# Performance work log

Measured on AMD Instinct MI355X. Metric: run time of the kernel, lower is better.

## Reference

```python
import jax, jax.numpy as jnp
import numpy as np

B, T = 64, 2048          # batch, encoder max steps
E, A, P = 256, 128, 128  # embedding_dim, attention_dim, prenet_dim
R, D, H = 1024, 1024, 256  # attention_rnn_dim, decoder_rnn_dim, hidden_dim
F, K = 32, 31            # location n_filters, kernel_size
PAD = (K - 1) // 2
NEG_INF = -1e30  # stands in for -inf; softmax-safe in fp32/bf16


def lstm_cell(x, h, c, W_ih, W_hh, b_ih, b_hh):
    # torch.nn.LSTMCell gate order: i, f, g, o
    gates = x @ W_ih.T + h @ W_hh.T + (b_ih + b_hh)
    i, f, g, o = jnp.split(gates, 4, axis=-1)
    c2 = jax.nn.sigmoid(f) * c + jax.nn.sigmoid(i) * jnp.tanh(g)
    h2 = jax.nn.sigmoid(o) * jnp.tanh(c2)
    return h2, c2


def setup_inputs() -> dict:
    key = jax.random.key(0)
    ks = jax.random.split(key, 30)
    n = jax.random.normal
    s = 0.02  # weight scale
    inp = {
        "last_frame": n(ks[0], (B, P)),
        "att_h": n(ks[1], (B, R)) * 0.1,
        "att_c": n(ks[2], (B, R)) * 0.1,
        "att_w": jax.random.uniform(ks[3], (B, T)) / T,
        "att_w_cum": jax.random.uniform(ks[4], (B, T)),
        "att_ctx": n(ks[5], (B, E)) * 0.1,
        "dec_h": n(ks[6], (B, D)) * 0.1,
        "dec_c": n(ks[7], (B, D)) * 0.1,
        "memory": n(ks[8], (B, T, E)),
        "processed_memory": n(ks[9], (B, T, A)) * 0.1,
        # attention LSTMCell (input = embedding_dim + prenet_dim = 384)
        "W_ih_a": n(ks[10], (4 * R, E + P)) * s,
        "W_hh_a": n(ks[11], (4 * R, R)) * s,
        "b_ih_a": n(ks[12], (4 * R,)) * s,
        "b_hh_a": n(ks[13], (4 * R,)) * s,
        # attention layer
        "W_q": n(ks[14], (A, R)) * s,
        "W_v": n(ks[15], (1, A)) * s,
        "W_loc": n(ks[16], (F, 2, K)) * s,   # Conv1d(2 -> F, k=31), no bias
        "W_lfc": n(ks[17], (A, F)) * s,
        # decoder LSTMCell (input = attention_rnn_dim + embedding_dim = 1280)
        "W_ih_d": n(ks[18], (4 * D, R + E)) * s,
        "W_hh_d": n(ks[19], (4 * D, D)) * s,
        "b_ih_d": n(ks[20], (4 * D,)) * s,
        "b_hh_d": n(ks[21], (4 * D,)) * s,
        # output heads
        "W_proj": n(ks[22], (H, D + E)) * s,
        "b_proj": n(ks[23], (H,)) * s,
        "W_gate": n(ks[24], (1, D + E)) * s,
        "b_gate": n(ks[25], (1,)) * s,
        "mask": jax.random.randint(ks[26], (B, T), 0, 2).astype(bool),
    }
    return inp


def reference(last_frame, att_h, att_c, att_w, att_w_cum, att_ctx, dec_h, dec_c,
              memory, processed_memory,
              W_ih_a, W_hh_a, b_ih_a, b_hh_a,
              W_q, W_v, W_loc, W_lfc,
              W_ih_d, W_hh_d, b_ih_d, b_hh_d,
              W_proj, b_proj, W_gate, b_gate, mask):
    # ---- attention RNN step (dropout = identity at eval) ----
    attention_in = jnp.concatenate([last_frame, att_ctx], axis=-1)  # [B, P+E]
    ah, ac = lstm_cell(attention_in, att_h, att_c, W_ih_a, W_hh_a, b_ih_a, b_hh_a)

    # ---- location-sensitive attention ----
    aw_cat = jnp.stack([att_w, att_w_cum], axis=1)  # [B, 2, T]
    loc = jax.lax.conv_general_dilated(
        aw_cat, W_loc, window_strides=(1,), padding=[(PAD, PAD)],
        dimension_numbers=('NCH', 'OIH', 'NCH'))  # [B, F, T]
    loc = jnp.einsum('bft,af->bta', loc, W_lfc)    # LocationLayer fc, [B, T, A]

    pq = (ah @ W_q.T)[:, None, :]                   # processed query [B, 1, A]
    energies = jnp.tanh(pq + processed_memory + loc) @ W_v[0]  # [B, T]
    energies = jnp.where(mask, NEG_INF, energies)
    weights = jax.nn.softmax(energies, axis=1)      # [B, T]
    ctx = jnp.einsum('bt,bte->be', weights, memory)  # [B, E]

    # ---- decoder RNN step ----
    decoder_in = jnp.concatenate([ah, ctx], axis=-1)  # [B, R+E]
    dh, dc = lstm_cell(decoder_in, dec_h, dec_c, W_ih_d, W_hh_d, b_ih_d, b_hh_d)

    dhac = jnp.concatenate([dh, ctx], axis=1)         # [B, D+E]
    decoder_output = dhac @ W_proj.T + b_proj          # [B, H]
    stop_prediction = dhac @ W_gate.T + b_gate         # [B, 1]
    return decoder_output, stop_prediction, weights[:, None, :]  # [B, 1, T]
```

## Files before the change

### kernel.cpp

```cpp
#include <hip/hip_runtime.h>
#include <stdint.h>

typedef unsigned short u16;
typedef __attribute__((ext_vector_type(8))) u16 u16x8;
typedef __attribute__((ext_vector_type(8))) __bf16 bf16x8;
typedef __attribute__((ext_vector_type(4))) float f32x4;

#define L2E 1.4426950408889634f

__device__ __forceinline__ float bf2f(u16 u) {
  union { unsigned i; float f; } v; v.i = ((unsigned)u) << 16; return v.f;
}
__device__ __forceinline__ u16 f2bf_rne(float f) {
  union { float f; unsigned u; } v; v.f = f;
  const unsigned r = v.u + 0x7FFFu + ((v.u >> 16) & 1u);
  return (u16)(r >> 16);
}
__device__ __forceinline__ bf16x8 ldb(const u16* p) {
  u16x8 v = *reinterpret_cast<const u16x8*>(p);
  return __builtin_bit_cast(bf16x8, v);
}
__device__ __forceinline__ void split8t(const float* p, bf16x8& h, bf16x8& l) {
  const float4 v0 = *reinterpret_cast<const float4*>(p);
  const float4 v1 = *reinterpret_cast<const float4*>(p + 4);
  const float f[8] = {v0.x, v0.y, v0.z, v0.w, v1.x, v1.y, v1.z, v1.w};
  u16x8 hu, lu;
#pragma unroll
  for (int i = 0; i < 8; ++i) {
    union { float f; unsigned u; } a; a.f = f[i];
    hu[i] = (u16)(a.u >> 16);
    union { float f; unsigned u; } hf; hf.u = a.u & 0xFFFF0000u;
    union { float f; unsigned u; } lo; lo.f = f[i] - hf.f;
    lu[i] = (u16)(lo.u >> 16);
  }
  h = __builtin_bit_cast(bf16x8, hu);
  l = __builtin_bit_cast(bf16x8, lu);
}
__device__ __forceinline__ f32x4 mfma16(bf16x8 a, bf16x8 b, f32x4 c) {
  return __builtin_amdgcn_mfma_f32_16x16x32_bf16(a, b, c, 0, 0, 0);
}
__device__ __forceinline__ float sigm(float x) {
  return 1.0f / (1.0f + exp2f(-L2E * x));
}
__device__ __forceinline__ float tanh_(float x) {
  return 1.0f - 2.0f / (1.0f + exp2f(2.0f * L2E * x));
}

__global__ __launch_bounds__(128) void k0_prep(
    const float* __restrict__ Wloc, const float* __restrict__ Wlfc,
    u16* __restrict__ w2b)
{
  const int k = blockIdx.x, a = threadIdx.x;
  float v = 0.0f;
  if (k < 62) {
    const int c = (k >= 31) ? 1 : 0, dk = k - c * 31;
    for (int f = 0; f < 32; ++f)
      v += Wlfc[a * 32 + f] * Wloc[f * 62 + c * 31 + dk];
  }
  w2b[a * 64 + k] = f2bf_rne(v);
}

#define KSA 8
__global__ __launch_bounds__(256) void k1_gemm(
    const float* __restrict__ lf, const float* __restrict__ actx,
    const float* __restrict__ ah_in,
    const float* __restrict__ Wih, const float* __restrict__ Whh,
    float* __restrict__ gates)
{
  const int tid = threadIdx.x;
  const int g = tid >> 6, lane = tid & 63, quad = lane >> 4, l16 = lane & 15;
  const int jb = blockIdx.x * 16, ks = blockIdx.y;
  const int n = g * 1024 + jb + l16;
  const int s0 = (ks * 44) / KSA, s1 = ((ks + 1) * 44) / KSA;
  f32x4 acc[4] = {{0,0,0,0},{0,0,0,0},{0,0,0,0},{0,0,0,0}};
  for (int s = s0; s < s1; ++s) {
    const int kb = s * 32, k = kb + quad * 8;
    const float* bp = (k < 384) ? (Wih + n * 384 + k) : (Whh + n * 1024 + (k - 384));
    bf16x8 b_h, b_l; split8t(bp, b_h, b_l);
#pragma unroll
    for (int mt = 0; mt < 4; ++mt) {
      const int mA = mt * 16 + l16;
      const float* ap;
      if (k < 128)      ap = lf    + mA * 128  + k;
      else if (k < 384) ap = actx  + mA * 256  + (k - 128);
      else              ap = ah_in + mA * 1024 + (k - 384);
      bf16x8 a_h, a_l; split8t(ap, a_h, a_l);
      acc[mt] = mfma16(a_h, b_h, acc[mt]);
      acc[mt] = mfma16(a_h, b_l, acc[mt]);
      acc[mt] = mfma16(a_l, b_h, acc[mt]);
    }
  }
#pragma unroll
  for (int mt = 0; mt < 4; ++mt)
#pragma unroll
    for (int r = 0; r < 4; ++r)
      atomicAdd(&gates[(mt * 16 + quad * 4 + r) * 4096 + n], acc[mt][r]);
}

__global__ __launch_bounds__(256) void k1_epi(
    const float* __restrict__ gates, const float* __restrict__ ac_in,
    const float* __restrict__ bih, const float* __restrict__ bhh,
    float* __restrict__ ah_f, u16* __restrict__ xd)
{
  const int lin = blockIdx.x * 256 + threadIdx.x;
  const int m = lin >> 10, j = lin & 1023;
  const float pi = gates[m * 4096 + j]        + bih[j]        + bhh[j];
  const float pf = gates[m * 4096 + 1024 + j] + bih[1024 + j] + bhh[1024 + j];
  const float pg = gates[m * 4096 + 2048 + j] + bih[2048 + j] + bhh[2048 + j];
  const float po = gates[m * 4096 + 3072 + j] + bih[3072 + j] + bhh[3072 + j];
  const float c2 = sigm(pf) * ac_in[m * 1024 + j] + sigm(pi) * tanh_(pg);
  const float h2 = sigm(po) * tanh_(c2);
  ah_f[m * 1024 + j] = h2;
  xd[m * 1280 + j]   = f2bf_rne(h2);
}

__global__ __launch_bounds__(256) void k2a_pq(
    const float* __restrict__ ah_f, const float* __restrict__ Wq, float* __restrict__ pq)
{
  const int lane = threadIdx.x & 63;
  const int wid = blockIdx.x * 4 + (threadIdx.x >> 6);
  const int a = wid & 127, bg = wid >> 7;
  float s[4] = {0, 0, 0, 0};
  for (int k = lane; k < 1024; k += 64) {
    const float wq = Wq[a * 1024 + k];
#pragma unroll
    for (int i = 0; i < 4; ++i) s[i] += wq * ah_f[(bg * 4 + i) * 1024 + k];
  }
#pragma unroll
  for (int i = 0; i < 4; ++i) {
    float v = s[i];
    for (int off = 1; off < 64; off <<= 1) v += __shfl_xor(v, off, 64);
    if (lane == 0) pq[(bg * 4 + i) * 128 + a] = v;
  }
}

__global__ __launch_bounds__(256) void k2_energy(
    const float* __restrict__ aw, const float* __restrict__ awc,
    const float* __restrict__ pm, const float* __restrict__ Wv,
    const float* __restrict__ pq, const u16* __restrict__ w2b,
    const int* __restrict__ msk, float* __restrict__ e_g)
{
  __shared__ __align__(16) u16 awin[2][64];
  __shared__ __align__(16) u16 pms[32 * 128];
  __shared__ __align__(16) u16 w2s[128 * 64];
  __shared__ float wvs[128];
  __shared__ float pqs[128];
  __shared__ float es[32];
  const int b = blockIdx.y, t0 = blockIdx.x * 32, tid = threadIdx.x;

  if (tid < 128) {
    const int c = tid >> 6, ii = tid & 63;
    const int t = t0 - 15 + ii;
    float v = 0.0f;
    if (ii < 62 && t >= 0 && t < 2048) v = (c ? awc : aw)[b * 2048 + t];
    awin[c][ii] = f2bf_rne(v);
    wvs[tid] = Wv[tid];
    pqs[tid] = pq[b * 128 + tid];
  }
  if (tid < 32) es[tid] = 0.0f;
  {
    const float* src = pm + (size_t)b * 262144 + (size_t)t0 * 128;
    const int i = tid * 16;
#pragma unroll
    for (int q = 0; q < 4; ++q) {
      const float4 v = *reinterpret_cast<const float4*>(&src[i + q * 4]);
      pms[i + q * 4 + 0] = f2bf_rne(v.x);
      pms[i + q * 4 + 1] = f2bf_rne(v.y);
      pms[i + q * 4 + 2] = f2bf_rne(v.z);
      pms[i + q * 4 + 3] = f2bf_rne(v.w);
    }
  }
  {
    const int i = tid * 32;
#pragma unroll
    for (int q = 0; q < 4; ++q)
      *reinterpret_cast<u16x8*>(&w2s[i + q * 8]) = *reinterpret_cast<const u16x8*>(&w2b[i + q * 8]);
  }
  __syncthreads();

  const int w = tid >> 6, lane = tid & 63, quad = lane >> 4, l16 = lane & 15;
  const int mt = w & 1, ng = w >> 1;
  f32x4 acc[4] = {{0,0,0,0},{0,0,0,0},{0,0,0,0},{0,0,0,0}};
#pragma unroll
  for (int ksx = 0; ksx < 2; ++ksx) {
    bf16x8 af;
    const int m = mt * 16 + l16;
#pragma unroll
    for (int jj = 0; jj < 8; ++jj) {
      const int k = ksx * 32 + quad * 8 + jj;
      u16 v = 0;
      if (k < 62) { const int c = (k >= 31) ? 1 : 0; const int dk = k - c * 31; v = awin[c][m + dk]; }
      af[jj] = __builtin_bit_cast(__bf16, v);
    }
#pragma unroll
    for (int p = 0; p < 4; ++p) {
      const int a = (ng * 4 + p) * 16 + l16;
      bf16x8 bfr = *reinterpret_cast<const bf16x8*>(&w2s[a * 64 + ksx * 32 + quad * 8]);
      acc[p] = mfma16(af, bfr, acc[p]);
    }
  }
#pragma unroll
  for (int r = 0; r < 4; ++r) {
    const int tl = mt * 16 + quad * 4 + r;
    float part = 0.0f;
#pragma unroll
    for (int p = 0; p < 4; ++p) {
      const int a = (ng * 4 + p) * 16 + l16;
      const float x = pqs[a] + bf2f(pms[tl * 128 + a]) + acc[p][r];
      part += wvs[a] * tanh_(x);
    }
    part += __shfl_xor(part, 1, 64);
    part += __shfl_xor(part, 2, 64);
    part += __shfl_xor(part, 4, 64);
    part += __shfl_xor(part, 8, 64);
    if (l16 == 0) atomicAdd(&es[tl], part);
  }
  __syncthreads();
  if (tid < 32) {
    const int t = t0 + tid;
    e_g[b * 2048 + t] = msk[b * 2048 + t] ? -1e30f : es[tid];
  }
}

__global__ __launch_bounds__(256) void k3a_softmax(
    const float* __restrict__ e_g, float* __restrict__ w_f, float* __restrict__ out_w)
{
  const int b = blockIdx.x, tid = threadIdx.x;
  __shared__ float red[4];
  float v[8];
  float mx = -3.0e38f;
#pragma unroll
  for (int i = 0; i < 8; ++i) { v[i] = e_g[b * 2048 + tid + i * 256]; mx = fmaxf(mx, v[i]); }
  for (int off = 1; off < 64; off <<= 1) mx = fmaxf(mx, __shfl_xor(mx, off, 64));
  if ((tid & 63) == 0) red[tid >> 6] = mx;
  __syncthreads();
  mx = fmaxf(fmaxf(red[0], red[1]), fmaxf(red[2], red[3]));
  float ex[8], s = 0.0f;
#pragma unroll
  for (int i = 0; i < 8; ++i) { ex[i] = exp2f((v[i] - mx) * L2E); s += ex[i]; }
  for (int off = 1; off < 64; off <<= 1) s += __shfl_xor(s, off, 64);
  __syncthreads();
  if ((tid & 63) == 0) red[tid >> 6] = s;
  __syncthreads();
  const float rs = 1.0f / (red[0] + red[1] + red[2] + red[3]);
#pragma unroll
  for (int i = 0; i < 8; ++i) {
    const int t = tid + i * 256;
    const float wv = ex[i] * rs;
    w_f[b * 2048 + t]   = wv;
    out_w[b * 2048 + t] = wv;
  }
}

__global__ __launch_bounds__(256) void k3b_ctx(
    const float* __restrict__ w_f, const float* __restrict__ mem, float* __restrict__ ctx)
{
  const int b = blockIdx.y, tc = blockIdx.x, tid = threadIdx.x;
  const int w = tid >> 6, lane = tid & 63;
  __shared__ float wsm[256];
  __shared__ float red[4][256];
  wsm[tid] = w_f[b * 2048 + tc * 256 + tid];
  __syncthreads();
  const float* mp = mem + (size_t)b * 524288 + ((size_t)tc * 256 + w * 64) * 256 + lane * 4;
  f32x4 acc = {0, 0, 0, 0};
#pragma unroll 4
  for (int t = 0; t < 64; ++t) {
    const float wt = wsm[w * 64 + t];
    const float4 v = *reinterpret_cast<const float4*>(mp + (size_t)t * 256);
    acc[0] += wt * v.x; acc[1] += wt * v.y; acc[2] += wt * v.z; acc[3] += wt * v.w;
  }
#pragma unroll
  for (int i = 0; i < 4; ++i) red[w][lane * 4 + i] = acc[i];
  __syncthreads();
  const float s = red[0][tid] + red[1][tid] + red[2][tid] + red[3][tid];
  atomicAdd(&ctx[b * 256 + tid], s);
}

__global__ __launch_bounds__(256) void k3c_cvt(
    const float* __restrict__ ctx, u16* __restrict__ xd, u16* __restrict__ dhac)
{
  const int b = blockIdx.x, e = threadIdx.x;
  const u16 v = f2bf_rne(ctx[b * 256 + e]);
  xd[b * 1280 + 1024 + e]   = v;
  dhac[b * 1280 + 1024 + e] = v;
}

__global__ __launch_bounds__(256) void k4_gemm(
    const u16* __restrict__ xd, const float* __restrict__ dh_in,
    const float* __restrict__ Wih, const float* __restrict__ Whh,
    float* __restrict__ gates)
{
  const int tid = threadIdx.x;
  const int g = tid >> 6, lane = tid & 63, quad = lane >> 4, l16 = lane & 15;
  const int jb = blockIdx.x * 16, ks = blockIdx.y;
  const int n = g * 1024 + jb + l16;
  const int kb0 = ks * 256, kb1 = kb0 + 256;
  f32x4 acc[4] = {{0,0,0,0},{0,0,0,0},{0,0,0,0},{0,0,0,0}};
  for (int kb = kb0; kb < kb1; kb += 32) {
    const int k = kb + quad * 8;
    const float* bp = (k < 1280) ? (Wih + n * 1280 + k) : (Whh + n * 1024 + (k - 1280));
    bf16x8 b_h, b_l; split8t(bp, b_h, b_l);
    if (k < 1280) {
#pragma unroll
      for (int mt = 0; mt < 4; ++mt) {
        bf16x8 a_h = ldb(xd + (mt * 16 + l16) * 1280 + k);
        acc[mt] = mfma16(a_h, b_h, acc[mt]);
        acc[mt] = mfma16(a_h, b_l, acc[mt]);
      }
    } else {
#pragma unroll
      for (int mt = 0; mt < 4; ++mt) {
        bf16x8 a_h, a_l; split8t(dh_in + (mt * 16 + l16) * 1024 + (k - 1280), a_h, a_l);
        acc[mt] = mfma16(a_h, b_h, acc[mt]);
        acc[mt] = mfma16(a_h, b_l, acc[mt]);
        acc[mt] = mfma16(a_l, b_h, acc[mt]);
      }
    }
  }
#pragma unroll
  for (int mt = 0; mt < 4; ++mt)
#pragma unroll
    for (int r = 0; r < 4; ++r)
      atomicAdd(&gates[(mt * 16 + quad * 4 + r) * 4096 + n], acc[mt][r]);
}

__global__ __launch_bounds__(256) void k4_epi(
    const float* __restrict__ gates, const float* __restrict__ dc_in,
    const float* __restrict__ bih, const float* __restrict__ bhh,
    u16* __restrict__ dhac)
{
  const int lin = blockIdx.x * 256 + threadIdx.x;
  const int m = lin >> 10, j = lin & 1023;
  const float pi = gates[m * 4096 + j]        + bih[j]        + bhh[j];
  const float pf = gates[m * 4096 + 1024 + j] + bih[1024 + j] + bhh[1024 + j];
  const float pg = gates[m * 4096 + 2048 + j] + bih[2048 + j] + bhh[2048 + j];
  const float po = gates[m * 4096 + 3072 + j] + bih[3072 + j] + bhh[3072 + j];
  const float c2 = sigm(pf) * dc_in[m * 1024 + j] + sigm(pi) * tanh_(pg);
  const float h2 = sigm(po) * tanh_(c2);
  dhac[m * 1280 + j] = f2bf_rne(h2);
}

__global__ __launch_bounds__(256) void k5_gemm(
    const u16* __restrict__ dhac, const float* __restrict__ Wp,
    float* __restrict__ proj)
{
  const int tid = threadIdx.x;
  const int w = tid >> 6, lane = tid & 63, quad = lane >> 4, l16 = lane & 15;
  const int n = blockIdx.x * 64 + w * 16 + l16, ks = blockIdx.y;
  const int kb0 = ks * 64;
  f32x4 acc[4] = {{0,0,0,0},{0,0,0,0},{0,0,0,0},{0,0,0,0}};
#pragma unroll
  for (int kb = kb0; kb < kb0 + 64; kb += 32) {
    const int k = kb + quad * 8;
    bf16x8 b_h, b_l; split8t(Wp + n * 1280 + k, b_h, b_l);
#pragma unroll
    for (int mt = 0; mt < 4; ++mt) {
      bf16x8 af = ldb(dhac + (mt * 16 + l16) * 1280 + k);
      acc[mt] = mfma16(af, b_h, acc[mt]);
      acc[mt] = mfma16(af, b_l, acc[mt]);
    }
  }
#pragma unroll
  for (int mt = 0; mt < 4; ++mt)
#pragma unroll
    for (int r = 0; r < 4; ++r)
      atomicAdd(&proj[(mt * 16 + quad * 4 + r) * 256 + n], acc[mt][r]);
}

__global__ __launch_bounds__(256) void k5_epi(
    const float* __restrict__ proj, const float* __restrict__ bp,
    const u16* __restrict__ dhac, const float* __restrict__ Wg,
    const float* __restrict__ bg, float* __restrict__ out)
{
  const int tid = threadIdx.x;
  if (blockIdx.x < 64) {
    const int m = blockIdx.x;
    out[m * 256 + tid] = proj[m * 256 + tid] + bp[tid];
  } else {
    const int w = tid >> 6, lane = tid & 63;
    const int bb = (blockIdx.x - 64) * 4 + w;
    float s = 0.0f;
    for (int k = lane; k < 1280; k += 64) s += bf2f(dhac[bb * 1280 + k]) * Wg[k];
    for (int off = 1; off < 64; off <<= 1) s += __shfl_xor(s, off, 64);
    if (lane == 0) out[16384 + bb] = s + bg[0];
  }
}

extern "C" void kernel_launch(void* const* d_in, const int* in_sizes, int n_in,
                              void* d_out, int out_size, void* d_ws, size_t ws_size,
                              hipStream_t stream)
{
  const float* lf    = (const float*)d_in[0];
  const float* ah0   = (const float*)d_in[1];
  const float* ac0   = (const float*)d_in[2];
  const float* aw    = (const float*)d_in[3];
  const float* awc   = (const float*)d_in[4];
  const float* actx  = (const float*)d_in[5];
  const float* dh0   = (const float*)d_in[6];
  const float* dc0   = (const float*)d_in[7];
  const float* mem   = (const float*)d_in[8];
  const float* pm    = (const float*)d_in[9];
  const float* Wih_a = (const float*)d_in[10];
  const float* Whh_a = (const float*)d_in[11];
  const float* bih_a = (const float*)d_in[12];
  const float* bhh_a = (const float*)d_in[13];
  const float* Wq    = (const float*)d_in[14];
  const float* Wv    = (const float*)d_in[15];
  const float* Wloc  = (const float*)d_in[16];
  const float* Wlfc  = (const float*)d_in[17];
  const float* Wih_d = (const float*)d_in[18];
  const float* Whh_d = (const float*)d_in[19];
  const float* bih_d = (const float*)d_in[20];
  const float* bhh_d = (const float*)d_in[21];
  const float* Wp    = (const float*)d_in[22];
  const float* bp    = (const float*)d_in[23];
  const float* Wg    = (const float*)d_in[24];
  const float* bg    = (const float*)d_in[25];
  const int* msk     = (const int*)d_in[26];

  float* wsf     = (float*)d_ws;
  float* gates_a = wsf;
  float* gates_d = wsf + 262144;
  float* proj    = wsf + 524288;
  float* ctx     = wsf + 540672;
  float* ah_f    = wsf + 557056;
  float* pq      = wsf + 622592;
  float* e_g     = wsf + 630784;
  float* w_f     = wsf + 761856;
  u16*  xd       = (u16*)(wsf + 892928);
  u16*  dhac     = xd + 81920;
  u16*  w2b      = dhac + 81920;

  float* out   = (float*)d_out;
  float* out_w = out + 16448;

  hipMemsetAsync(d_ws, 0, 557056 * sizeof(float), stream);

  k0_prep    <<<64, 128, 0, stream>>>(Wloc, Wlfc, w2b);
  k1_gemm    <<<dim3(64, KSA), 256, 0, stream>>>(lf, actx, ah0, Wih_a, Whh_a, gates_a);
  k1_epi     <<<256, 256, 0, stream>>>(gates_a, ac0, bih_a, bhh_a, ah_f, xd);
  k2a_pq     <<<512, 256, 0, stream>>>(ah_f, Wq, pq);
  k2_energy  <<<dim3(64, 64), 256, 0, stream>>>(aw, awc, pm, Wv, pq, w2b, msk, e_g);
  k3a_softmax<<<64, 256, 0, stream>>>(e_g, w_f, out_w);
  k3b_ctx    <<<dim3(8, 64), 256, 0, stream>>>(w_f, mem, ctx);
  k3c_cvt    <<<64, 256, 0, stream>>>(ctx, xd, dhac);
  k4_gemm    <<<dim3(64, 9), 256, 0, stream>>>(xd, dh0, Wih_d, Whh_d, gates_d);
  k4_epi     <<<256, 256, 0, stream>>>(gates_d, dc0, bih_d, bhh_d, dhac);
  k5_gemm    <<<dim3(4, 20), 256, 0, stream>>>(dhac, Wp, proj);
  k5_epi     <<<80, 256, 0, stream>>>(proj, bp, dhac, Wg, bg, out);
}
```

Measured before the change: 400.3 us.

## Fuse all decoder stages into one cooperative persistent kernel with grid barriers

Replaces the twelve separate launches and the memset with a single cooperative persistent kernel. Stages are separated by a software grid barrier, and the workspace is zeroed inside the kernel. The decoder GEMM now converts ctx to bf16 inline, and the xd layout is shrunk. This removes per-launch overhead and the gaps between kernels. In exchange, occupancy is limited by the union of all shared-memory buffers, and grid-strided loops may leave some stages with fewer blocks than before, such as the energy stage's 4096 blocks.

```diff
diff --git a/kernel.cpp b/kernel.cpp
--- a/kernel.cpp
+++ b/kernel.cpp
@@ -7,6 +7,7 @@
 typedef __attribute__((ext_vector_type(4))) float f32x4;
 
 #define L2E 1.4426950408889634f
+#define NBLK_MAX 512
 
 __device__ __forceinline__ float bf2f(u16 u) {
   union { unsigned i; float f; } v; v.i = ((unsigned)u) << 16; return v.f;
@@ -36,6 +37,15 @@
   h = __builtin_bit_cast(bf16x8, hu);
   l = __builtin_bit_cast(bf16x8, lu);
 }
+__device__ __forceinline__ bf16x8 cvt8_rne(const float* p) {
+  const float4 v0 = *reinterpret_cast<const float4*>(p);
+  const float4 v1 = *reinterpret_cast<const float4*>(p + 4);
+  const float f[8] = {v0.x, v0.y, v0.z, v0.w, v1.x, v1.y, v1.z, v1.w};
+  u16x8 u;
+#pragma unroll
+  for (int i = 0; i < 8; ++i) u[i] = f2bf_rne(f[i]);
+  return __builtin_bit_cast(bf16x8, u);
+}
 __device__ __forceinline__ f32x4 mfma16(bf16x8 a, bf16x8 b, f32x4 c) {
   return __builtin_amdgcn_mfma_f32_16x16x32_bf16(a, b, c, 0, 0, 0);
 }
@@ -46,343 +56,362 @@
   return 1.0f - 2.0f / (1.0f + exp2f(2.0f * L2E * x));
 }
 
-__global__ __launch_bounds__(128) void k0_prep(
-    const float* __restrict__ Wloc, const float* __restrict__ Wlfc,
-    u16* __restrict__ w2b)
+__device__ __align__(128) unsigned g_cnt = 0;
+__device__ __align__(128) unsigned g_gen = 0;
+
+__device__ __forceinline__ void gbar() {
+  __syncthreads();
+  if (threadIdx.x == 0) {
+    const unsigned tgt = gridDim.x;
+    const unsigned g = __hip_atomic_load(&g_gen, __ATOMIC_RELAXED, __HIP_MEMORY_SCOPE_AGENT);
+    const unsigned a = __hip_atomic_fetch_add(&g_cnt, 1u, __ATOMIC_ACQ_REL, __HIP_MEMORY_SCOPE_AGENT);
+    if (a == tgt - 1u) {
+      __hip_atomic_store(&g_cnt, 0u, __ATOMIC_RELAXED, __HIP_MEMORY_SCOPE_AGENT);
+      __hip_atomic_store(&g_gen, g + 1u, __ATOMIC_RELEASE, __HIP_MEMORY_SCOPE_AGENT);
+    } else {
+      while (__hip_atomic_load(&g_gen, __ATOMIC_RELAXED, __HIP_MEMORY_SCOPE_AGENT) == g)
+        __builtin_amdgcn_s_sleep(2);
+      (void)__hip_atomic_load(&g_gen, __ATOMIC_ACQUIRE, __HIP_MEMORY_SCOPE_AGENT);
+    }
+  }
+  __syncthreads();
+}
+
+struct MArgs {
+  const float *lf, *ah0, *ac0, *aw, *awc, *actx, *dh0, *dc0, *mem, *pm;
+  const float *Wih_a, *Whh_a, *bih_a, *bhh_a;
+  const float *Wq, *Wv, *Wloc, *Wlfc;
+  const float *Wih_d, *Whh_d, *bih_d, *bhh_d;
+  const float *Wp, *bp, *Wg, *bg;
+  const int *msk;
+  float *wsf;
+  float *out;
+};
+
+__global__ __launch_bounds__(256, 2) void mega(MArgs A)
 {
-  const int k = blockIdx.x, a = threadIdx.x;
-  float v = 0.0f;
-  if (k < 62) {
-    const int c = (k >= 31) ? 1 : 0, dk = k - c * 31;
-    for (int f = 0; f < 32; ++f)
-      v += Wlfc[a * 32 + f] * Wloc[f * 62 + c * 31 + dk];
-  }
-  w2b[a * 64 + k] = f2bf_rne(v);
-}
-
-#define KSA 8
-__global__ __launch_bounds__(256) void k1_gemm(
-    const float* __restrict__ lf, const float* __restrict__ actx,
-    const float* __restrict__ ah_in,
-    const float* __restrict__ Wih, const float* __restrict__ Whh,
-    float* __restrict__ gates)
-{
-  const int tid = threadIdx.x;
-  const int g = tid >> 6, lane = tid & 63, quad = lane >> 4, l16 = lane & 15;
-  const int jb = blockIdx.x * 16, ks = blockIdx.y;
-  const int n = g * 1024 + jb + l16;
-  const int s0 = (ks * 44) / KSA, s1 = ((ks + 1) * 44) / KSA;
-  f32x4 acc[4] = {{0,0,0,0},{0,0,0,0},{0,0,0,0},{0,0,0,0}};
-  for (int s = s0; s < s1; ++s) {
-    const int kb = s * 32, k = kb + quad * 8;
-    const float* bp = (k < 384) ? (Wih + n * 384 + k) : (Whh + n * 1024 + (k - 384));
-    bf16x8 b_h, b_l; split8t(bp, b_h, b_l);
-#pragma unroll
-    for (int mt = 0; mt < 4; ++mt) {
-      const int mA = mt * 16 + l16;
-      const float* ap;
-      if (k < 128)      ap = lf    + mA * 128  + k;
-      else if (k < 384) ap = actx  + mA * 256  + (k - 128);
-      else              ap = ah_in + mA * 1024 + (k - 384);
-      bf16x8 a_h, a_l; split8t(ap, a_h, a_l);
-      acc[mt] = mfma16(a_h, b_h, acc[mt]);
-      acc[mt] = mfma16(a_h, b_l, acc[mt]);
-      acc[mt] = mfma16(a_l, b_h, acc[mt]);
-    }
-  }
-#pragma unroll
-  for (int mt = 0; mt < 4; ++mt)
-#pragma unroll
-    for (int r = 0; r < 4; ++r)
-      atomicAdd(&gates[(mt * 16 + quad * 4 + r) * 4096 + n], acc[mt][r]);
-}
-
-__global__ __launch_bounds__(256) void k1_epi(
-    const float* __restrict__ gates, const float* __restrict__ ac_in,
-    const float* __restrict__ bih, const float* __restrict__ bhh,
-    float* __restrict__ ah_f, u16* __restrict__ xd)
-{
-  const int lin = blockIdx.x * 256 + threadIdx.x;
-  const int m = lin >> 10, j = lin & 1023;
-  const float pi = gates[m * 4096 + j]        + bih[j]        + bhh[j];
-  const float pf = gates[m * 4096 + 1024 + j] + bih[1024 + j] + bhh[1024 + j];
-  const float pg = gates[m * 4096 + 2048 + j] + bih[2048 + j] + bhh[2048 + j];
-  const float po = gates[m * 4096 + 3072 + j] + bih[3072 + j] + bhh[3072 + j];
-  const float c2 = sigm(pf) * ac_in[m * 1024 + j] + sigm(pi) * tanh_(pg);
-  const float h2 = sigm(po) * tanh_(c2);
-  ah_f[m * 1024 + j] = h2;
-  xd[m * 1280 + j]   = f2bf_rne(h2);
-}
-
-__global__ __launch_bounds__(256) void k2a_pq(
-    const float* __restrict__ ah_f, const float* __restrict__ Wq, float* __restrict__ pq)
-{
-  const int lane = threadIdx.x & 63;
-  const int wid = blockIdx.x * 4 + (threadIdx.x >> 6);
-  const int a = wid & 127, bg = wid >> 7;
-  float s[4] = {0, 0, 0, 0};
-  for (int k = lane; k < 1024; k += 64) {
-    const float wq = Wq[a * 1024 + k];
-#pragma unroll
-    for (int i = 0; i < 4; ++i) s[i] += wq * ah_f[(bg * 4 + i) * 1024 + k];
-  }
-#pragma unroll
-  for (int i = 0; i < 4; ++i) {
-    float v = s[i];
-    for (int off = 1; off < 64; off <<= 1) v += __shfl_xor(v, off, 64);
-    if (lane == 0) pq[(bg * 4 + i) * 128 + a] = v;
-  }
-}
-
-__global__ __launch_bounds__(256) void k2_energy(
-    const float* __restrict__ aw, const float* __restrict__ awc,
-    const float* __restrict__ pm, const float* __restrict__ Wv,
-    const float* __restrict__ pq, const u16* __restrict__ w2b,
-    const int* __restrict__ msk, float* __restrict__ e_g)
-{
+  const int tid  = threadIdx.x;
+  const int bid  = blockIdx.x;
+  const int gd   = gridDim.x;
+  const int gtid = bid * 256 + tid;
+  const int gs   = gd * 256;
+  const int w    = tid >> 6, lane = tid & 63, quad = lane >> 4, l16 = lane & 15;
+
+  float* gates_a = A.wsf;
+  float* gates_d = A.wsf + 262144;
+  float* proj    = A.wsf + 524288;
+  float* ctx     = A.wsf + 540672;
+  float* ah_f    = A.wsf + 557056;
+  float* pq      = A.wsf + 622592;
+  float* e_g     = A.wsf + 630784;
+  u16*  xd       = (u16*)(A.wsf + 761856);
+  u16*  dhac     = (u16*)(A.wsf + 794624);
+  u16*  w2b      = (u16*)(A.wsf + 835584);
+  float* out     = A.out;
+  float* out_w   = A.out + 16448;
+
   __shared__ __align__(16) u16 awin[2][64];
   __shared__ __align__(16) u16 pms[32 * 128];
   __shared__ __align__(16) u16 w2s[128 * 64];
   __shared__ float wvs[128];
   __shared__ float pqs[128];
   __shared__ float es[32];
-  const int b = blockIdx.y, t0 = blockIdx.x * 32, tid = threadIdx.x;
-
-  if (tid < 128) {
-    const int c = tid >> 6, ii = tid & 63;
-    const int t = t0 - 15 + ii;
-    float v = 0.0f;
-    if (ii < 62 && t >= 0 && t < 2048) v = (c ? awc : aw)[b * 2048 + t];
-    awin[c][ii] = f2bf_rne(v);
-    wvs[tid] = Wv[tid];
-    pqs[tid] = pq[b * 128 + tid];
-  }
-  if (tid < 32) es[tid] = 0.0f;
+  __shared__ float red4[4];
+  __shared__ float wsm[256];
+  __shared__ float redc[4][256];
+
   {
-    const float* src = pm + (size_t)b * 262144 + (size_t)t0 * 128;
-    const int i = tid * 16;
-#pragma unroll
-    for (int q = 0; q < 4; ++q) {
-      const float4 v = *reinterpret_cast<const float4*>(&src[i + q * 4]);
-      pms[i + q * 4 + 0] = f2bf_rne(v.x);
-      pms[i + q * 4 + 1] = f2bf_rne(v.y);
-      pms[i + q * 4 + 2] = f2bf_rne(v.z);
-      pms[i + q * 4 + 3] = f2bf_rne(v.w);
-    }
-  }
-  {
-    const int i = tid * 32;
-#pragma unroll
-    for (int q = 0; q < 4; ++q)
-      *reinterpret_cast<u16x8*>(&w2s[i + q * 8]) = *reinterpret_cast<const u16x8*>(&w2b[i + q * 8]);
-  }
-  __syncthreads();
-
-  const int w = tid >> 6, lane = tid & 63, quad = lane >> 4, l16 = lane & 15;
-  const int mt = w & 1, ng = w >> 1;
-  f32x4 acc[4] = {{0,0,0,0},{0,0,0,0},{0,0,0,0},{0,0,0,0}};
-#pragma unroll
-  for (int ksx = 0; ksx < 2; ++ksx) {
-    bf16x8 af;
-    const int m = mt * 16 + l16;
-#pragma unroll
-    for (int jj = 0; jj < 8; ++jj) {
-      const int k = ksx * 32 + quad * 8 + jj;
-      u16 v = 0;
-      if (k < 62) { const int c = (k >= 31) ? 1 : 0; const int dk = k - c * 31; v = awin[c][m + dk]; }
-      af[jj] = __builtin_bit_cast(__bf16, v);
-    }
-#pragma unroll
-    for (int p = 0; p < 4; ++p) {
-      const int a = (ng * 4 + p) * 16 + l16;
-      bf16x8 bfr = *reinterpret_cast<const bf16x8*>(&w2s[a * 64 + ksx * 32 + quad * 8]);
-      acc[p] = mfma16(af, bfr, acc[p]);
-    }
-  }
-#pragma unroll
-  for (int r = 0; r < 4; ++r) {
-    const int tl = mt * 16 + quad * 4 + r;
-    float part = 0.0f;
-#pragma unroll
-    for (int p = 0; p < 4; ++p) {
-      const int a = (ng * 4 + p) * 16 + l16;
-      const float x = pqs[a] + bf2f(pms[tl * 128 + a]) + acc[p][r];
-      part += wvs[a] * tanh_(x);
-    }
-    part += __shfl_xor(part, 1, 64);
-    part += __shfl_xor(part, 2, 64);
-    part += __shfl_xor(part, 4, 64);
-    part += __shfl_xor(part, 8, 64);
-    if (l16 == 0) atomicAdd(&es[tl], part);
-  }
-  __syncthreads();
-  if (tid < 32) {
-    const int t = t0 + tid;
-    e_g[b * 2048 + t] = msk[b * 2048 + t] ? -1e30f : es[tid];
-  }
-}
-
-__global__ __launch_bounds__(256) void k3a_softmax(
-    const float* __restrict__ e_g, float* __restrict__ w_f, float* __restrict__ out_w)
-{
-  const int b = blockIdx.x, tid = threadIdx.x;
-  __shared__ float red[4];
-  float v[8];
-  float mx = -3.0e38f;
-#pragma unroll
-  for (int i = 0; i < 8; ++i) { v[i] = e_g[b * 2048 + tid + i * 256]; mx = fmaxf(mx, v[i]); }
-  for (int off = 1; off < 64; off <<= 1) mx = fmaxf(mx, __shfl_xor(mx, off, 64));
-  if ((tid & 63) == 0) red[tid >> 6] = mx;
-  __syncthreads();
-  mx = fmaxf(fmaxf(red[0], red[1]), fmaxf(red[2], red[3]));
-  float ex[8], s = 0.0f;
-#pragma unroll
-  for (int i = 0; i < 8; ++i) { ex[i] = exp2f((v[i] - mx) * L2E); s += ex[i]; }
-  for (int off = 1; off < 64; off <<= 1) s += __shfl_xor(s, off, 64);
-  __syncthreads();
-  if ((tid & 63) == 0) red[tid >> 6] = s;
-  __syncthreads();
-  const float rs = 1.0f / (red[0] + red[1] + red[2] + red[3]);
-#pragma unroll
-  for (int i = 0; i < 8; ++i) {
-    const int t = tid + i * 256;
-    const float wv = ex[i] * rs;
-    w_f[b * 2048 + t]   = wv;
-    out_w[b * 2048 + t] = wv;
-  }
-}
-
-__global__ __launch_bounds__(256) void k3b_ctx(
-    const float* __restrict__ w_f, const float* __restrict__ mem, float* __restrict__ ctx)
-{
-  const int b = blockIdx.y, tc = blockIdx.x, tid = threadIdx.x;
-  const int w = tid >> 6, lane = tid & 63;
-  __shared__ float wsm[256];
-  __shared__ float red[4][256];
-  wsm[tid] = w_f[b * 2048 + tc * 256 + tid];
-  __syncthreads();
-  const float* mp = mem + (size_t)b * 524288 + ((size_t)tc * 256 + w * 64) * 256 + lane * 4;
-  f32x4 acc = {0, 0, 0, 0};
-#pragma unroll 4
-  for (int t = 0; t < 64; ++t) {
-    const float wt = wsm[w * 64 + t];
-    const float4 v = *reinterpret_cast<const float4*>(mp + (size_t)t * 256);
-    acc[0] += wt * v.x; acc[1] += wt * v.y; acc[2] += wt * v.z; acc[3] += wt * v.w;
-  }
-#pragma unroll
-  for (int i = 0; i < 4; ++i) red[w][lane * 4 + i] = acc[i];
-  __syncthreads();
-  const float s = red[0][tid] + red[1][tid] + red[2][tid] + red[3][tid];
-  atomicAdd(&ctx[b * 256 + tid], s);
-}
-
-__global__ __launch_bounds__(256) void k3c_cvt(
-    const float* __restrict__ ctx, u16* __restrict__ xd, u16* __restrict__ dhac)
-{
-  const int b = blockIdx.x, e = threadIdx.x;
-  const u16 v = f2bf_rne(ctx[b * 256 + e]);
-  xd[b * 1280 + 1024 + e]   = v;
-  dhac[b * 1280 + 1024 + e] = v;
-}
-
-__global__ __launch_bounds__(256) void k4_gemm(
-    const u16* __restrict__ xd, const float* __restrict__ dh_in,
-    const float* __restrict__ Wih, const float* __restrict__ Whh,
-    float* __restrict__ gates)
-{
-  const int tid = threadIdx.x;
-  const int g = tid >> 6, lane = tid & 63, quad = lane >> 4, l16 = lane & 15;
-  const int jb = blockIdx.x * 16, ks = blockIdx.y;
-  const int n = g * 1024 + jb + l16;
-  const int kb0 = ks * 256, kb1 = kb0 + 256;
-  f32x4 acc[4] = {{0,0,0,0},{0,0,0,0},{0,0,0,0},{0,0,0,0}};
-  for (int kb = kb0; kb < kb1; kb += 32) {
-    const int k = kb + quad * 8;
-    const float* bp = (k < 1280) ? (Wih + n * 1280 + k) : (Whh + n * 1024 + (k - 1280));
-    bf16x8 b_h, b_l; split8t(bp, b_h, b_l);
-    if (k < 1280) {
+    f32x4* z = (f32x4*)A.wsf;
+    for (int i = gtid; i < 139264; i += gs) z[i] = (f32x4){0.f, 0.f, 0.f, 0.f};
+    for (int lin = gtid; lin < 8192; lin += gs) {
+      const int a = lin >> 6, k = lin & 63;
+      float v = 0.0f;
+      if (k < 62) {
+        const int c = (k >= 31) ? 1 : 0, dk = k - c * 31;
+        for (int f = 0; f < 32; ++f)
+          v += A.Wlfc[a * 32 + f] * A.Wloc[f * 62 + c * 31 + dk];
+      }
+      w2b[a * 64 + k] = f2bf_rne(v);
+    }
+  }
+  gbar();
+
+  for (int vb = bid; vb < 512; vb += gd) {
+    const int g = w;
+    const int jt = vb & 63, ks = vb >> 6;
+    const int n = g * 1024 + jt * 16 + l16;
+    const int s0 = (ks * 44) / 8, s1 = ((ks + 1) * 44) / 8;
+    f32x4 acc[4] = {{0,0,0,0},{0,0,0,0},{0,0,0,0},{0,0,0,0}};
+    for (int s = s0; s < s1; ++s) {
+      const int kb = s * 32, k = kb + quad * 8;
+      const float* bp = (k < 384) ? (A.Wih_a + n * 384 + k) : (A.Whh_a + n * 1024 + (k - 384));
+      bf16x8 b_h, b_l; split8t(bp, b_h, b_l);
 #pragma unroll
       for (int mt = 0; mt < 4; ++mt) {
-        bf16x8 a_h = ldb(xd + (mt * 16 + l16) * 1280 + k);
-        acc[mt] = mfma16(a_h, b_h, acc[mt]);
-        acc[mt] = mfma16(a_h, b_l, acc[mt]);
-      }
-    } else {
-#pragma unroll
-      for (int mt = 0; mt < 4; ++mt) {
-        bf16x8 a_h, a_l; split8t(dh_in + (mt * 16 + l16) * 1024 + (k - 1280), a_h, a_l);
+        const int mA = mt * 16 + l16;
+        const float* ap;
+        if (k < 128)      ap = A.lf   + mA * 128  + k;
+        else if (k < 384) ap = A.actx + mA * 256  + (k - 128);
+        else              ap = A.ah0  + mA * 1024 + (k - 384);
+        bf16x8 a_h, a_l; split8t(ap, a_h, a_l);
         acc[mt] = mfma16(a_h, b_h, acc[mt]);
         acc[mt] = mfma16(a_h, b_l, acc[mt]);
         acc[mt] = mfma16(a_l, b_h, acc[mt]);
       }
     }
-  }
-#pragma unroll
-  for (int mt = 0; mt < 4; ++mt)
-#pragma unroll
-    for (int r = 0; r < 4; ++r)
-      atomicAdd(&gates[(mt * 16 + quad * 4 + r) * 4096 + n], acc[mt][r]);
-}
-
-__global__ __launch_bounds__(256) void k4_epi(
-    const float* __restrict__ gates, const float* __restrict__ dc_in,
-    const float* __restrict__ bih, const float* __restrict__ bhh,
-    u16* __restrict__ dhac)
-{
-  const int lin = blockIdx.x * 256 + threadIdx.x;
-  const int m = lin >> 10, j = lin & 1023;
-  const float pi = gates[m * 4096 + j]        + bih[j]        + bhh[j];
-  const float pf = gates[m * 4096 + 1024 + j] + bih[1024 + j] + bhh[1024 + j];
-  const float pg = gates[m * 4096 + 2048 + j] + bih[2048 + j] + bhh[2048 + j];
-  const float po = gates[m * 4096 + 3072 + j] + bih[3072 + j] + bhh[3072 + j];
-  const float c2 = sigm(pf) * dc_in[m * 1024 + j] + sigm(pi) * tanh_(pg);
-  const float h2 = sigm(po) * tanh_(c2);
-  dhac[m * 1280 + j] = f2bf_rne(h2);
-}
-
-__global__ __launch_bounds__(256) void k5_gemm(
-    const u16* __restrict__ dhac, const float* __restrict__ Wp,
-    float* __restrict__ proj)
-{
-  const int tid = threadIdx.x;
-  const int w = tid >> 6, lane = tid & 63, quad = lane >> 4, l16 = lane & 15;
-  const int n = blockIdx.x * 64 + w * 16 + l16, ks = blockIdx.y;
-  const int kb0 = ks * 64;
-  f32x4 acc[4] = {{0,0,0,0},{0,0,0,0},{0,0,0,0},{0,0,0,0}};
-#pragma unroll
-  for (int kb = kb0; kb < kb0 + 64; kb += 32) {
-    const int k = kb + quad * 8;
-    bf16x8 b_h, b_l; split8t(Wp + n * 1280 + k, b_h, b_l);
-#pragma unroll
-    for (int mt = 0; mt < 4; ++mt) {
-      bf16x8 af = ldb(dhac + (mt * 16 + l16) * 1280 + k);
-      acc[mt] = mfma16(af, b_h, acc[mt]);
-      acc[mt] = mfma16(af, b_l, acc[mt]);
-    }
-  }
-#pragma unroll
-  for (int mt = 0; mt < 4; ++mt)
-#pragma unroll
-    for (int r = 0; r < 4; ++r)
-      atomicAdd(&proj[(mt * 16 + quad * 4 + r) * 256 + n], acc[mt][r]);
-}
-
-__global__ __launch_bounds__(256) void k5_epi(
-    const float* __restrict__ proj, const float* __restrict__ bp,
-    const u16* __restrict__ dhac, const float* __restrict__ Wg,
-    const float* __restrict__ bg, float* __restrict__ out)
-{
-  const int tid = threadIdx.x;
-  if (blockIdx.x < 64) {
-    const int m = blockIdx.x;
-    out[m * 256 + tid] = proj[m * 256 + tid] + bp[tid];
-  } else {
-    const int w = tid >> 6, lane = tid & 63;
-    const int bb = (blockIdx.x - 64) * 4 + w;
-    float s = 0.0f;
-    for (int k = lane; k < 1280; k += 64) s += bf2f(dhac[bb * 1280 + k]) * Wg[k];
+#pragma unroll
+    for (int mt = 0; mt < 4; ++mt)
+#pragma unroll
+      for (int r = 0; r < 4; ++r)
+        atomicAdd(&gates_a[(mt * 16 + quad * 4 + r) * 4096 + n], acc[mt][r]);
+  }
+  gbar();
+
+  for (int lin = gtid; lin < 65536; lin += gs) {
+    const int m = lin >> 10, j = lin & 1023;
+    const float pi = gates_a[m * 4096 + j]        + A.bih_a[j]        + A.bhh_a[j];
+    const float pf = gates_a[m * 4096 + 1024 + j] + A.bih_a[1024 + j] + A.bhh_a[1024 + j];
+    const float pg = gates_a[m * 4096 + 2048 + j] + A.bih_a[2048 + j] + A.bhh_a[2048 + j];
+    const float po = gates_a[m * 4096 + 3072 + j] + A.bih_a[3072 + j] + A.bhh_a[3072 + j];
+    const float c2 = sigm(pf) * A.ac0[m * 1024 + j] + sigm(pi) * tanh_(pg);
+    const float h2 = sigm(po) * tanh_(c2);
+    ah_f[m * 1024 + j] = h2;
+    xd[m * 1024 + j]   = f2bf_rne(h2);
+  }
+  gbar();
+
+  for (int vb = bid; vb < 512; vb += gd) {
+    const int wid = vb * 4 + w;
+    const int a = wid & 127, bg = wid >> 7;
+    float s4[4] = {0, 0, 0, 0};
+    for (int k = lane; k < 1024; k += 64) {
+      const float wq = A.Wq[a * 1024 + k];
+#pragma unroll
+      for (int i = 0; i < 4; ++i) s4[i] += wq * ah_f[(bg * 4 + i) * 1024 + k];
+    }
+#pragma unroll
+    for (int i = 0; i < 4; ++i) {
+      float v = s4[i];
+      for (int off = 1; off < 64; off <<= 1) v += __shfl_xor(v, off, 64);
+      if (lane == 0) pq[(bg * 4 + i) * 128 + a] = v;
+    }
+  }
+  gbar();
+
+  {
+    const int i0 = tid * 32;
+#pragma unroll
+    for (int q = 0; q < 4; ++q)
+      *reinterpret_cast<u16x8*>(&w2s[i0 + q * 8]) = *reinterpret_cast<const u16x8*>(&w2b[i0 + q * 8]);
+  }
+  for (int vb = bid; vb < 512; vb += gd) {
+    const int b = vb >> 3, tch = vb & 7;
+    if (tid < 128) { wvs[tid] = A.Wv[tid]; pqs[tid] = pq[b * 128 + tid]; }
+    const int mt_ = w & 1, ng = w >> 1;
+    for (int it = 0; it < 8; ++it) {
+      const int t0 = (tch * 8 + it) * 32;
+      __syncthreads();
+      if (tid < 128) {
+        const int c = tid >> 6, ii = tid & 63;
+        const int t = t0 - 15 + ii;
+        float v = 0.0f;
+        if (ii < 62 && t >= 0 && t < 2048) v = (c ? A.awc : A.aw)[b * 2048 + t];
+        awin[c][ii] = f2bf_rne(v);
+      }
+      if (tid < 32) es[tid] = 0.0f;
+      {
+        const float* src = A.pm + (size_t)b * 262144 + (size_t)t0 * 128;
+        const int i = tid * 16;
+#pragma unroll
+        for (int q = 0; q < 4; ++q) {
+          const float4 v = *reinterpret_cast<const float4*>(&src[i + q * 4]);
+          pms[i + q * 4 + 0] = f2bf_rne(v.x);
+          pms[i + q * 4 + 1] = f2bf_rne(v.y);
+          pms[i + q * 4 + 2] = f2bf_rne(v.z);
+          pms[i + q * 4 + 3] = f2bf_rne(v.w);
+        }
+      }
+      __syncthreads();
+      f32x4 acc[4] = {{0,0,0,0},{0,0,0,0},{0,0,0,0},{0,0,0,0}};
+#pragma unroll
+      for (int ksx = 0; ksx < 2; ++ksx) {
+        bf16x8 af;
+        const int m2 = mt_ * 16 + l16;
+#pragma unroll
+        for (int jj = 0; jj < 8; ++jj) {
+          const int k = ksx * 32 + quad * 8 + jj;
+          u16 v = 0;
+          if (k < 62) { const int c = (k >= 31) ? 1 : 0; const int dk = k - c * 31; v = awin[c][m2 + dk]; }
+          af[jj] = __builtin_bit_cast(__bf16, v);
+        }
+#pragma unroll
+        for (int p = 0; p < 4; ++p) {
+          const int a = (ng * 4 + p) * 16 + l16;
+          bf16x8 bfr = *reinterpret_cast<const bf16x8*>(&w2s[a * 64 + ksx * 32 + quad * 8]);
+          acc[p] = mfma16(af, bfr, acc[p]);
+        }
+      }
+#pragma unroll
+      for (int r = 0; r < 4; ++r) {
+        const int tl = mt_ * 16 + quad * 4 + r;
+        float part = 0.0f;
+#pragma unroll
+        for (int p = 0; p < 4; ++p) {
+          const int a = (ng * 4 + p) * 16 + l16;
+          const float x = pqs[a] + bf2f(pms[tl * 128 + a]) + acc[p][r];
+          part += wvs[a] * tanh_(x);
+        }
+        part += __shfl_xor(part, 1, 64);
+        part += __shfl_xor(part, 2, 64);
+        part += __shfl_xor(part, 4, 64);
+        part += __shfl_xor(part, 8, 64);
+        if (l16 == 0) atomicAdd(&es[tl], part);
+      }
+      __syncthreads();
+      if (tid < 32) {
+        const int t = t0 + tid;
+        e_g[b * 2048 + t] = A.msk[b * 2048 + t] ? -1e30f : es[tid];
+      }
+    }
+  }
+  gbar();
+
+  for (int vb = bid; vb < 512; vb += gd) {
+    const int b = vb >> 3, tc = vb & 7;
+    __syncthreads();
+    float v8[8];
+    float mx = -3.0e38f;
+#pragma unroll
+    for (int i = 0; i < 8; ++i) { v8[i] = e_g[b * 2048 + tid + i * 256]; mx = fmaxf(mx, v8[i]); }
+    for (int off = 1; off < 64; off <<= 1) mx = fmaxf(mx, __shfl_xor(mx, off, 64));
+    if ((tid & 63) == 0) red4[tid >> 6] = mx;
+    __syncthreads();
+    mx = fmaxf(fmaxf(red4[0], red4[1]), fmaxf(red4[2], red4[3]));
+    float ex[8], s = 0.0f;
+#pragma unroll
+    for (int i = 0; i < 8; ++i) { ex[i] = exp2f((v8[i] - mx) * L2E); s += ex[i]; }
     for (int off = 1; off < 64; off <<= 1) s += __shfl_xor(s, off, 64);
-    if (lane == 0) out[16384 + bb] = s + bg[0];
+    __syncthreads();
+    if ((tid & 63) == 0) red4[tid >> 6] = s;
+    __syncthreads();
+    const float rs = 1.0f / (red4[0] + red4[1] + red4[2] + red4[3]);
+    float exc = 0.0f;
+#pragma unroll
+    for (int i = 0; i < 8; ++i) if (i == tc) exc = ex[i];
+    const float wv = exc * rs;
+    out_w[b * 2048 + tc * 256 + tid] = wv;
+    wsm[tid] = wv;
+    __syncthreads();
+    const float* mp = A.mem + (size_t)b * 524288 + ((size_t)tc * 256 + w * 64) * 256 + lane * 4;
+    f32x4 acc = {0, 0, 0, 0};
+#pragma unroll 4
+    for (int t = 0; t < 64; ++t) {
+      const float wt = wsm[w * 64 + t];
+      const float4 v = *reinterpret_cast<const float4*>(mp + (size_t)t * 256);
+      acc[0] += wt * v.x; acc[1] += wt * v.y; acc[2] += wt * v.z; acc[3] += wt * v.w;
+    }
+#pragma unroll
+    for (int i = 0; i < 4; ++i) redc[w][lane * 4 + i] = acc[i];
+    __syncthreads();
+    const float s2 = redc[0][tid] + redc[1][tid] + redc[2][tid] + redc[3][tid];
+    atomicAdd(&ctx[b * 256 + tid], s2);
+  }
+  gbar();
+
+  for (int vb = bid; vb < 512; vb += gd) {
+    const int g = w;
+    const int jt = vb & 63, ks = vb >> 6;
+    const int n = g * 1024 + jt * 16 + l16;
+    f32x4 acc[4] = {{0,0,0,0},{0,0,0,0},{0,0,0,0},{0,0,0,0}};
+    for (int s = ks * 9; s < ks * 9 + 9; ++s) {
+      const int kb = s * 32, k = kb + quad * 8;
+      const float* bp = (k < 1280) ? (A.Wih_d + n * 1280 + k) : (A.Whh_d + n * 1024 + (k - 1280));
+      bf16x8 b_h, b_l; split8t(bp, b_h, b_l);
+      if (k < 1024) {
+#pragma unroll
+        for (int mt = 0; mt < 4; ++mt) {
+          bf16x8 a_h = ldb(xd + (mt * 16 + l16) * 1024 + k);
+          acc[mt] = mfma16(a_h, b_h, acc[mt]);
+          acc[mt] = mfma16(a_h, b_l, acc[mt]);
+        }
+      } else if (k < 1280) {
+#pragma unroll
+        for (int mt = 0; mt < 4; ++mt) {
+          bf16x8 a_h = cvt8_rne(ctx + (mt * 16 + l16) * 256 + (k - 1024));
+          acc[mt] = mfma16(a_h, b_h, acc[mt]);
+          acc[mt] = mfma16(a_h, b_l, acc[mt]);
+        }
+      } else {
+#pragma unroll
+        for (int mt = 0; mt < 4; ++mt) {
+          bf16x8 a_h, a_l; split8t(A.dh0 + (mt * 16 + l16) * 1024 + (k - 1280), a_h, a_l);
+          acc[mt] = mfma16(a_h, b_h, acc[mt]);
+          acc[mt] = mfma16(a_h, b_l, acc[mt]);
+          acc[mt] = mfma16(a_l, b_h, acc[mt]);
+        }
+      }
+    }
+#pragma unroll
+    for (int mt = 0; mt < 4; ++mt)
+#pragma unroll
+      for (int r = 0; r < 4; ++r)
+        atomicAdd(&gates_d[(mt * 16 + quad * 4 + r) * 4096 + n], acc[mt][r]);
+  }
+  gbar();
+
+  for (int lin = gtid; lin < 81920; lin += gs) {
+    if (lin < 65536) {
+      const int m = lin >> 10, j = lin & 1023;
+      const float pi = gates_d[m * 4096 + j]        + A.bih_d[j]        + A.bhh_d[j];
+      const float pf = gates_d[m * 4096 + 1024 + j] + A.bih_d[1024 + j] + A.bhh_d[1024 + j];
+      const float pg = gates_d[m * 4096 + 2048 + j] + A.bih_d[2048 + j] + A.bhh_d[2048 + j];
+      const float po = gates_d[m * 4096 + 3072 + j] + A.bih_d[3072 + j] + A.bhh_d[3072 + j];
+      const float c2 = sigm(pf) * A.dc0[m * 1024 + j] + sigm(pi) * tanh_(pg);
+      const float h2 = sigm(po) * tanh_(c2);
+      dhac[m * 1280 + j] = f2bf_rne(h2);
+    } else {
+      const int lin2 = lin - 65536;
+      const int b2 = lin2 >> 8, e = lin2 & 255;
+      dhac[b2 * 1280 + 1024 + e] = f2bf_rne(ctx[b2 * 256 + e]);
+    }
+  }
+  gbar();
+
+  for (int vb = bid; vb < 96; vb += gd) {
+    if (vb < 80) {
+      const int xb = vb & 3, ks = vb >> 2;
+      const int n = xb * 64 + w * 16 + l16;
+      const int kb0 = ks * 64;
+      f32x4 acc[4] = {{0,0,0,0},{0,0,0,0},{0,0,0,0},{0,0,0,0}};
+#pragma unroll
+      for (int kb = kb0; kb < kb0 + 64; kb += 32) {
+        const int k = kb + quad * 8;
+        bf16x8 b_h, b_l; split8t(A.Wp + n * 1280 + k, b_h, b_l);
+#pragma unroll
+        for (int mt = 0; mt < 4; ++mt) {
+          bf16x8 af = ldb(dhac + (mt * 16 + l16) * 1280 + k);
+          acc[mt] = mfma16(af, b_h, acc[mt]);
+          acc[mt] = mfma16(af, b_l, acc[mt]);
+        }
+      }
+#pragma unroll
+      for (int mt = 0; mt < 4; ++mt)
+#pragma unroll
+        for (int r = 0; r < 4; ++r)
+          atomicAdd(&proj[(mt * 16 + quad * 4 + r) * 256 + n], acc[mt][r]);
+    } else {
+      const int bb = (vb - 80) * 4 + w;
+      float s = 0.0f;
+      for (int k = lane; k < 1280; k += 64) s += bf2f(dhac[bb * 1280 + k]) * A.Wg[k];
+      for (int off = 1; off < 64; off <<= 1) s += __shfl_xor(s, off, 64);
+      if (lane == 0) out[16384 + bb] = s + A.bg[0];
+    }
+  }
+  gbar();
+
+  for (int lin = gtid; lin < 16384; lin += gs) {
+    const int m = lin >> 8, e = lin & 255;
+    out[m * 256 + e] = proj[m * 256 + e] + A.bp[e];
   }
 }
 
@@ -390,62 +419,48 @@
                               void* d_out, int out_size, void* d_ws, size_t ws_size,
                               hipStream_t stream)
 {
-  const float* lf    = (const float*)d_in[0];
-  const float* ah0   = (const float*)d_in[1];
-  const float* ac0   = (const float*)d_in[2];
-  const float* aw    = (const float*)d_in[3];
-  const float* awc   = (const float*)d_in[4];
-  const float* actx  = (const float*)d_in[5];
-  const float* dh0   = (const float*)d_in[6];
-  const float* dc0   = (const float*)d_in[7];
-  const float* mem   = (const float*)d_in[8];
-  const float* pm    = (const float*)d_in[9];
-  const float* Wih_a = (const float*)d_in[10];
-  const float* Whh_a = (const float*)d_in[11];
-  const float* bih_a = (const float*)d_in[12];
-  const float* bhh_a = (const float*)d_in[13];
-  const float* Wq    = (const float*)d_in[14];
-  const float* Wv    = (const float*)d_in[15];
-  const float* Wloc  = (const float*)d_in[16];
-  const float* Wlfc  = (const float*)d_in[17];
-  const float* Wih_d = (const float*)d_in[18];
-  const float* Whh_d = (const float*)d_in[19];
-  const float* bih_d = (const float*)d_in[20];
-  const float* bhh_d = (const float*)d_in[21];
-  const float* Wp    = (const float*)d_in[22];
-  const float* bp    = (const float*)d_in[23];
-  const float* Wg    = (const float*)d_in[24];
-  const float* bg    = (const float*)d_in[25];
-  const int* msk     = (const int*)d_in[26];
-
-  float* wsf     = (float*)d_ws;
-  float* gates_a = wsf;
-  float* gates_d = wsf + 262144;
-  float* proj    = wsf + 524288;
-  float* ctx     = wsf + 540672;
-  float* ah_f    = wsf + 557056;
-  float* pq      = wsf + 622592;
-  float* e_g     = wsf + 630784;
-  float* w_f     = wsf + 761856;
-  u16*  xd       = (u16*)(wsf + 892928);
-  u16*  dhac     = xd + 81920;
-  u16*  w2b      = dhac + 81920;
-
-  float* out   = (float*)d_out;
-  float* out_w = out + 16448;
-
-  hipMemsetAsync(d_ws, 0, 557056 * sizeof(float), stream);
-
-  k0_prep    <<<64, 128, 0, stream>>>(Wloc, Wlfc, w2b);
-  k1_gemm    <<<dim3(64, KSA), 256, 0, stream>>>(lf, actx, ah0, Wih_a, Whh_a, gates_a);
-  k1_epi     <<<256, 256, 0, stream>>>(gates_a, ac0, bih_a, bhh_a, ah_f, xd);
-  k2a_pq     <<<512, 256, 0, stream>>>(ah_f, Wq, pq);
-  k2_energy  <<<dim3(64, 64), 256, 0, stream>>>(aw, awc, pm, Wv, pq, w2b, msk, e_g);
-  k3a_softmax<<<64, 256, 0, stream>>>(e_g, w_f, out_w);
-  k3b_ctx    <<<dim3(8, 64), 256, 0, stream>>>(w_f, mem, ctx);
-  k3c_cvt    <<<64, 256, 0, stream>>>(ctx, xd, dhac);
-  k4_gemm    <<<dim3(64, 9), 256, 0, stream>>>(xd, dh0, Wih_d, Whh_d, gates_d);
-  k4_epi     <<<256, 256, 0, stream>>>(gates_d, dc0, bih_d, bhh_d, dhac);
-  k5_gemm    <<<dim3(4, 20), 256, 0, stream>>>(dhac, Wp, proj);
-  k5_epi     <<<80, 256, 0, stream>>>(proj, bp, dhac, Wg, bg, out);
-}
+  (void)in_sizes; (void)n_in; (void)out_size; (void)ws_size;
+  MArgs a;
+  a.lf    = (const float*)d_in[0];
+  a.ah0   = (const float*)d_in[1];
+  a.ac0   = (const float*)d_in[2];
+  a.aw    = (const float*)d_in[3];
+  a.awc   = (const float*)d_in[4];
+  a.actx  = (const float*)d_in[5];
+  a.dh0   = (const float*)d_in[6];
+  a.dc0   = (const float*)d_in[7];
+  a.mem   = (const float*)d_in[8];
+  a.pm    = (const float*)d_in[9];
+  a.Wih_a = (const float*)d_in[10];
+  a.Whh_a = (const float*)d_in[11];
+  a.bih_a = (const float*)d_in[12];
+  a.bhh_a = (const float*)d_in[13];
+  a.Wq    = (const float*)d_in[14];
+  a.Wv    = (const float*)d_in[15];
+  a.Wloc  = (const float*)d_in[16];
+  a.Wlfc  = (const float*)d_in[17];
+  a.Wih_d = (const float*)d_in[18];
+  a.Whh_d = (const float*)d_in[19];
+  a.bih_d = (const float*)d_in[20];
+  a.bhh_d = (const float*)d_in[21];
+  a.Wp    = (const float*)d_in[22];
+  a.bp    = (const float*)d_in[23];
+  a.Wg    = (const float*)d_in[24];
+  a.bg    = (const float*)d_in[25];
+  a.msk   = (const int*)d_in[26];
+  a.wsf   = (float*)d_ws;
+  a.out   = (float*)d_out;
+
+  static int nblk = 0;
+  if (nblk == 0) {
+    int occ = 0;
+    (void)hipOccupancyMaxActiveBlocksPerMultiprocessor(&occ, mega, 256, 0);
+    if (occ < 1) occ = 1;
+    nblk = occ * 256;
+    if (nblk > NBLK_MAX) nblk = NBLK_MAX;
+  }
+
+  void* params[] = { (void*)&a };
+  (void)hipLaunchCooperativeKernel((const void*)mega, dim3(nblk), dim3(256),
+                                   params, 0, stream);
+}
```

Result: slower. 589.0 us (+47.1%).
